# Optimization experiments

Measured on AMD Instinct MI355X. Metric: run time of the kernel, lower is better.

The kernel has to match this reference:

```python
import jax, jax.numpy as jnp
import numpy as np

B, H, W, C = 8, 64, 64, 256  # NHWC, SAGAN-style feature map


def setup_inputs() -> dict:
    key = jax.random.key(0)
    ks = jax.random.split(key, 10)
    d_qk, d_v = C // 8, C // 2
    sc = lambda fan_in: 1.0 / np.sqrt(fan_in)
    return {
        "x": jax.random.normal(ks[0], (B, H, W, C), dtype=jnp.float32),
        "Wf": jax.random.normal(ks[1], (C, d_qk), dtype=jnp.float32) * sc(C),
        "bf": jnp.zeros((d_qk,), dtype=jnp.float32),
        "Wg": jax.random.normal(ks[2], (C, d_qk), dtype=jnp.float32) * sc(C),
        "bg": jnp.zeros((d_qk,), dtype=jnp.float32),
        "Wh": jax.random.normal(ks[3], (C, d_v), dtype=jnp.float32) * sc(C),
        "bh": jnp.zeros((d_v,), dtype=jnp.float32),
        "Wo": jax.random.normal(ks[4], (d_v, C), dtype=jnp.float32) * sc(d_v),
        "bo": jnp.zeros((C,), dtype=jnp.float32),
        # original inits gamma=0.0 (identity fwd); use nonzero so fwd exercises attention
        "gamma": jnp.float32(0.5),
    }


def reference(x, Wf, bf, Wg, bg, Wh, bh, Wo, bo, gamma):
    b, h_, w_, c = x.shape
    n = h_ * w_
    xf = x.reshape(b, n, c)  # 1x1 convs are per-pixel GEMMs
    f = xf @ Wf + bf          # [B, N, C/8]  (keys)
    g = xf @ Wg + bg          # [B, N, C/8]  (queries)
    hv = xf @ Wh + bh         # [B, N, C/2]  (values)
    s = jnp.einsum('bnd,bmd->bnm', g, f)   # unscaled scores [B, N, N]
    beta = jax.nn.softmax(s, axis=-1)
    o = jnp.einsum('bnm,bmd->bnd', beta, hv)  # [B, N, C/2]
    o = o @ Wo + bo                           # output 1x1 conv -> [B, N, C]
    out = gamma * o + xf
    return out.reshape(b, h_, w_, c)
```

## Files before the change

### kernel.cpp

```cpp
#include <hip/hip_runtime.h>
#include <hip/hip_bf16.h>

#define NB   8
#define CC   256
#define NN   4096
#define NTOT (NB*NN)
#define DQK  32
#define DV   128

typedef __attribute__((ext_vector_type(8))) short bf16x8;
typedef __attribute__((ext_vector_type(4))) short s16x4;
typedef __attribute__((ext_vector_type(4))) float f32x4;
typedef __attribute__((ext_vector_type(16))) float f32x16;
typedef __attribute__((ext_vector_type(4))) float float4v;
typedef __attribute__((ext_vector_type(4))) unsigned int u32x4;

__device__ __forceinline__ short f2bf(float f) {
    __hip_bfloat16 h = __float2bfloat16(f);
    return *reinterpret_cast<short*>(&h);
}
__device__ __forceinline__ float bf2f(short s) {
    unsigned int u = ((unsigned int)(unsigned short)s) << 16;
    return __builtin_bit_cast(float, u);
}
__device__ __forceinline__ unsigned int cvtpk(float lo, float hi) {
    unsigned int r;
    asm("v_cvt_pk_bf16_f32 %0, %1, %2" : "=v"(r) : "v"(lo), "v"(hi));
    return r;
}
__device__ __forceinline__ void plswap(unsigned int &a, unsigned int &b) {
    asm("v_permlane32_swap_b32 %0, %1" : "+v"(a), "+v"(b));
}

#define OFF_F     0u
#define OFF_G     (2u<<20)
#define OFF_VT    (4u<<20)
#define OFF_OP    (12u<<20)
#define OFF_LS    (28u<<20)
#define OFF_WQKVT ((28u<<20)+(512u<<10))
#define OFF_WOT   (OFF_WQKVT + 192u*256u*2u)

__global__ __launch_bounds__(256) void prep_kernel(
    const float* __restrict__ Wf, const float* __restrict__ Wg,
    const float* __restrict__ Wh, const float* __restrict__ Wo,
    short* __restrict__ WqkvT, short* __restrict__ WoT)
{
    int idx = blockIdx.x * 256 + threadIdx.x;
    if (idx < 192 * 256) {
        int j = idx >> 8, k = idx & 255;
        float v = (j < 32) ? Wf[k * 32 + j]
                : (j < 64) ? Wg[k * 32 + (j - 32)]
                           : Wh[k * 128 + (j - 64)];
        WqkvT[j * 256 + k] = f2bf(v);
    }
    int i2 = idx - 192 * 256;
    if (i2 >= 0 && i2 < 256 * 128) {
        int c = i2 >> 7, d = i2 & 127;
        WoT[c * 128 + d] = f2bf(Wo[d * 256 + c]);
    }
}

__global__ __launch_bounds__(256) void proj_kernel(
    const float* __restrict__ x,
    const float* __restrict__ bf_, const float* __restrict__ bg_,
    const float* __restrict__ bh_,
    const short* __restrict__ WqkvT,
    short* __restrict__ fws, short* __restrict__ gws, short* __restrict__ vtile)
{
    __shared__ short hlds[128 * 72];

    int wid = threadIdx.x >> 6, lane = threadIdx.x & 63;
    int col16 = lane & 15, rq = lane >> 4;
    int bid = blockIdx.x;
    int sid = (bid & 7) * 64 + (bid >> 3);
    int nloc = wid * 16 + col16;
    int arow = sid * 64 + nloc;
    int b = sid >> 6, kt = sid & 63;

    f32x4 acc[12];
    #pragma unroll
    for (int i = 0; i < 12; ++i) acc[i] = (f32x4){0.f, 0.f, 0.f, 0.f};

    const float* xrow = x + (size_t)arow * CC;
    #pragma unroll
    for (int kk = 0; kk < 8; ++kk) {
        int k0 = kk * 32 + rq * 8;
        float4v u0 = *(const float4v*)(xrow + k0);
        float4v u1 = *(const float4v*)(xrow + k0 + 4);
        bf16x8 av;
        av[0]=f2bf(u0[0]); av[1]=f2bf(u0[1]); av[2]=f2bf(u0[2]); av[3]=f2bf(u0[3]);
        av[4]=f2bf(u1[0]); av[5]=f2bf(u1[1]); av[6]=f2bf(u1[2]); av[7]=f2bf(u1[3]);
        #pragma unroll
        for (int nf = 0; nf < 12; ++nf) {
            bf16x8 bv = *(const bf16x8*)(WqkvT + (nf * 16 + col16) * 256 + k0);
            acc[nf] = __builtin_amdgcn_mfma_f32_16x16x32_bf16(bv, av, acc[nf], 0, 0, 0);
        }
    }

    #pragma unroll
    for (int nf = 0; nf < 2; ++nf) {
        int c0 = nf * 16 + rq * 4;
        float4v b4 = *(const float4v*)(bf_ + c0);
        s16x4 v = { f2bf(acc[nf][0] + b4[0]), f2bf(acc[nf][1] + b4[1]),
                    f2bf(acc[nf][2] + b4[2]), f2bf(acc[nf][3] + b4[3]) };
        *(s16x4*)(fws + (size_t)arow * DQK + c0) = v;
    }
    #pragma unroll
    for (int nf = 2; nf < 4; ++nf) {
        int c0 = (nf - 2) * 16 + rq * 4;
        float4v b4 = *(const float4v*)(bg_ + c0);
        s16x4 v = { f2bf((acc[nf][0] + b4[0]) * 1.44269504089f),
                    f2bf((acc[nf][1] + b4[1]) * 1.44269504089f),
                    f2bf((acc[nf][2] + b4[2]) * 1.44269504089f),
                    f2bf((acc[nf][3] + b4[3]) * 1.44269504089f) };
        *(s16x4*)(gws + (size_t)arow * DQK + c0) = v;
    }

    #pragma unroll
    for (int nf = 4; nf < 12; ++nf) {
        int d0 = (nf - 4) * 16 + rq * 4;
        float4v b4 = *(const float4v*)(bh_ + d0);
        #pragma unroll
        for (int r = 0; r < 4; ++r)
            hlds[(d0 + r) * 72 + nloc] = f2bf(acc[nf][r] + b4[r]);
    }
    __syncthreads();

    int t = threadIdx.x;
    int l31 = t & 31, dt = (t >> 5) & 3, klh = t >> 7;
    int d = dt * 32 + l31;
    #pragma unroll
    for (int kslot = 0; kslot < 4; ++kslot) {
        bf16x8 v = *(const bf16x8*)(&hlds[d * 72 + kslot * 16 + klh * 8]);
        size_t addr = (((size_t)(b * 64 + kt) * 4 + kslot) * 2048)
                    + dt * 512 + klh * 256 + l31 * 8;
        *(bf16x8*)(vtile + addr) = v;
    }
}

__global__ __launch_bounds__(256, 4) void attn_kernel(
    const short* __restrict__ fws, const short* __restrict__ gws,
    const short* __restrict__ vtile, short* __restrict__ opart,
    float* __restrict__ lspart)
{
    __shared__ __align__(16) char smem[33280];

    int t = threadIdx.x;
    int wid = t >> 6, lane = t & 63;
    int l31 = lane & 31, lh = lane >> 5;
    int qh = wid >> 1, kh = wid & 1;

    int bid = blockIdx.x;
    int sid = (bid & 7) * 128 + (bid >> 3);
    int b = sid >> 7, rem = sid & 127;
    int ksh = rem >> 6, qt = rem & 63;
    int qbase = b * NN + qt * 64;
    int k0 = ksh * 32, kend = k0 + 32;

    const short* grow = gws + (size_t)(qbase + qh * 32 + l31) * DQK;
    bf16x8 gb0 = *(const bf16x8*)(grow + lh * 8);
    bf16x8 gb1 = *(const bf16x8*)(grow + 16 + lh * 8);

    int foff = (kh * 32 + l31) * DQK + lh * 8;
    const short* fS = fws + (size_t)b * NN * DQK;

    f32x16 oaccT[4], zero16;
    #pragma unroll
    for (int i = 0; i < 16; ++i) {
        zero16[i] = 0.f;
        oaccT[0][i] = 0.f; oaccT[1][i] = 0.f; oaccT[2][i] = 0.f; oaccT[3][i] = 0.f;
    }
    float lsum = 0.f;

    bf16x8 fc0 = *(const bf16x8*)(fS + (size_t)k0 * 2048 + foff);
    bf16x8 fc1 = *(const bf16x8*)(fS + (size_t)k0 * 2048 + foff + 16);

    for (int kb = k0; kb < kend; ++kb) {
        const short* fnp = fS + (size_t)(kb + 1) * 2048 + foff;
        bf16x8 fn0 = *(const bf16x8*)(fnp);
        bf16x8 fn1 = *(const bf16x8*)(fnp + 16);

        f32x16 s = __builtin_amdgcn_mfma_f32_32x32x16_bf16(fc0, gb0, zero16, 0, 0, 0);
        s = __builtin_amdgcn_mfma_f32_32x32x16_bf16(fc1, gb1, s, 0, 0, 0);

        unsigned int w[8];
        #pragma unroll
        for (int i = 0; i < 8; ++i) {
            float pa = __builtin_exp2f(s[2 * i]);
            float pb = __builtin_exp2f(s[2 * i + 1]);
            lsum += pa + pb;
            w[i] = cvtpk(pa, pb);
        }
        plswap(w[0], w[2]); plswap(w[1], w[3]);
        plswap(w[4], w[6]); plswap(w[5], w[7]);

        const short* vb_kb = vtile + (((size_t)(b * 64 + kb) * 4 + kh * 2) * 2048)
                           + (size_t)lane * 8;
        #pragma unroll
        for (int ks = 0; ks < 2; ++ks) {
            u32x4 pw = { w[ks * 4], w[ks * 4 + 1], w[ks * 4 + 2], w[ks * 4 + 3] };
            bf16x8 pb_ = __builtin_bit_cast(bf16x8, pw);
            #pragma unroll
            for (int dt = 0; dt < 4; ++dt) {
                bf16x8 va = *(const bf16x8*)(vb_kb + ks * 2048 + dt * 512);
                oaccT[dt] = __builtin_amdgcn_mfma_f32_32x32x16_bf16(va, pb_, oaccT[dt], 0, 0, 0);
            }
        }
        fc0 = fn0; fc1 = fn1;
    }

    lsum += __shfl_xor(lsum, 32);
    float* lsbuf = (float*)(&smem[32768]);
    if (lh == 0) lsbuf[(qh * 2 + kh) * 32 + l31] = lsum;
    __syncthreads();

    char* obuf = smem;
    if (kh == 1) {
        #pragma unroll
        for (int dt = 0; dt < 4; ++dt) {
            #pragma unroll
            for (int r = 0; r < 16; ++r) {
                int d = dt * 32 + (r & 3) + 8 * (r >> 2) + 4 * lh;
                int q = qh * 32 + l31;
                int byte = q * 512 + ((((d >> 2) ^ (q & 31)) << 4) | ((d & 3) << 2));
                *(float*)(obuf + byte) = oaccT[dt][r];
            }
        }
    }
    __syncthreads();
    if (kh == 0) {
        float tot = lsbuf[qh * 64 + l31] + lsbuf[qh * 64 + 32 + l31];
        if (lh == 0) lspart[(size_t)(qbase + qh * 32 + l31) * 2 + ksh] = tot;
        float iv = 1.f / tot;
        #pragma unroll
        for (int dt = 0; dt < 4; ++dt) {
            #pragma unroll
            for (int r = 0; r < 16; ++r) {
                int d = dt * 32 + (r & 3) + 8 * (r >> 2) + 4 * lh;
                int q = qh * 32 + l31;
                int byte = q * 512 + ((((d >> 2) ^ (q & 31)) << 4) | ((d & 3) << 2));
                float* p = (float*)(obuf + byte);
                *p = (*p + oaccT[dt][r]) * iv;
            }
        }
    }
    __syncthreads();
    {
        int q = t >> 2, dg = t & 3;
        size_t orow = ((size_t)(qbase + q) * 2 + ksh) * 128 + dg * 32;
        #pragma unroll
        for (int cc = 0; cc < 8; cc += 2) {
            int c0 = dg * 8 + cc;
            f32x4 u0 = *(const f32x4*)(obuf + q * 512 + (((c0 ^ (q & 31)) << 4)));
            f32x4 u1 = *(const f32x4*)(obuf + q * 512 + ((((c0 + 1) ^ (q & 31)) << 4)));
            bf16x8 ov;
            ov[0]=f2bf(u0[0]); ov[1]=f2bf(u0[1]); ov[2]=f2bf(u0[2]); ov[3]=f2bf(u0[3]);
            ov[4]=f2bf(u1[0]); ov[5]=f2bf(u1[1]); ov[6]=f2bf(u1[2]); ov[7]=f2bf(u1[3]);
            *(bf16x8*)(opart + orow + cc * 4) = ov;
        }
    }
}

__global__ __launch_bounds__(256) void out_kernel(
    const short* __restrict__ opart, const float* __restrict__ lspart,
    const short* __restrict__ WoT,
    const float* __restrict__ bo, const float* __restrict__ gamma,
    const float* __restrict__ x, float* __restrict__ out)
{
    int wid = threadIdx.x >> 6, lane = threadIdx.x & 63;
    int col16 = lane & 15, rq = lane >> 4;
    int bid = blockIdx.x;
    int sid = (bid & 7) * 128 + (bid >> 3);
    int rh = wid & 1, ch = wid >> 1;
    int arow = sid * 32 + rh * 16 + col16;

    float l0 = lspart[(size_t)arow * 2];
    float l1 = lspart[(size_t)arow * 2 + 1];
    float iv = 1.f / (l0 + l1);
    float w0 = l0 * iv, w1 = l1 * iv;

    const short* oprow = opart + (size_t)arow * 256;
    bf16x8 bfr[4];
    #pragma unroll
    for (int kk = 0; kk < 4; ++kk) {
        bf16x8 a0 = *(const bf16x8*)(oprow + kk * 32 + rq * 8);
        bf16x8 a1 = *(const bf16x8*)(oprow + 128 + kk * 32 + rq * 8);
        bf16x8 af;
        #pragma unroll
        for (int j = 0; j < 8; ++j)
            af[j] = f2bf(w0 * bf2f(a0[j]) + w1 * bf2f(a1[j]));
        bfr[kk] = af;
    }

    f32x4 acc[8];
    #pragma unroll
    for (int i = 0; i < 8; ++i) acc[i] = (f32x4){0.f, 0.f, 0.f, 0.f};

    #pragma unroll
    for (int nf = 0; nf < 8; ++nf) {
        int nt = ch * 8 + nf;
        #pragma unroll
        for (int kk = 0; kk < 4; ++kk) {
            bf16x8 wfr = *(const bf16x8*)(WoT + (nt * 16 + col16) * DV + kk * 32 + rq * 8);
            acc[nf] = __builtin_amdgcn_mfma_f32_16x16x32_bf16(wfr, bfr[kk], acc[nf], 0, 0, 0);
        }
    }

    float gm = gamma[0];
    const float* xrow = x + (size_t)arow * CC;
    float* orow_ = out + (size_t)arow * CC;
    #pragma unroll
    for (int nf = 0; nf < 8; ++nf) {
        int c0 = (ch * 8 + nf) * 16 + rq * 4;
        float4v bo4 = *(const float4v*)(bo + c0);
        float4v xv = *(const float4v*)(xrow + c0);
        float4v ov;
        #pragma unroll
        for (int r = 0; r < 4; ++r)
            ov[r] = gm * (acc[nf][r] + bo4[r]) + xv[r];
        *(float4v*)(orow_ + c0) = ov;
    }
}

extern "C" void kernel_launch(void* const* d_in, const int* in_sizes, int n_in,
                              void* d_out, int out_size, void* d_ws, size_t ws_size,
                              hipStream_t stream)
{
    const float* x     = (const float*)d_in[0];
    const float* Wf    = (const float*)d_in[1];
    const float* bf_   = (const float*)d_in[2];
    const float* Wg    = (const float*)d_in[3];
    const float* bg_   = (const float*)d_in[4];
    const float* Wh    = (const float*)d_in[5];
    const float* bh_   = (const float*)d_in[6];
    const float* Wo    = (const float*)d_in[7];
    const float* bo    = (const float*)d_in[8];
    const float* gamma = (const float*)d_in[9];

    char* ws = (char*)d_ws;
    short* fws   = (short*)(ws + OFF_F);
    short* gws   = (short*)(ws + OFF_G);
    short* vtile = (short*)(ws + OFF_VT);
    short* opart = (short*)(ws + OFF_OP);
    float* lsp   = (float*)(ws + OFF_LS);
    short* WqkvT = (short*)(ws + OFF_WQKVT);
    short* WoT   = (short*)(ws + OFF_WOT);
    float* out   = (float*)d_out;

    hipLaunchKernelGGL(prep_kernel, dim3(320), dim3(256), 0, stream, Wf, Wg, Wh, Wo, WqkvT, WoT);
    hipLaunchKernelGGL(proj_kernel, dim3(512), dim3(256), 0, stream,
                       x, bf_, bg_, bh_, WqkvT, fws, gws, vtile);
    hipLaunchKernelGGL(attn_kernel, dim3(1024), dim3(256), 0, stream, fws, gws, vtile, opart, lsp);
    hipLaunchKernelGGL(out_kernel, dim3(1024), dim3(256), 0, stream, opart, lsp, WoT, bo, gamma, x, out);
}
```

Measured before the change: 126.0 us.

## Split projection over 32-row tiles with column halves per wave; use packed bf16 converts

```diff
diff --git a/kernel.cpp b/kernel.cpp
--- a/kernel.cpp
+++ b/kernel.cpp
@@ -14,6 +14,7 @@
 typedef __attribute__((ext_vector_type(16))) float f32x16;
 typedef __attribute__((ext_vector_type(4))) float float4v;
 typedef __attribute__((ext_vector_type(4))) unsigned int u32x4;
+typedef __attribute__((ext_vector_type(2))) unsigned int u32x2;
 
 __device__ __forceinline__ short f2bf(float f) {
     __hip_bfloat16 h = __float2bfloat16(f);
@@ -67,19 +68,21 @@
     const short* __restrict__ WqkvT,
     short* __restrict__ fws, short* __restrict__ gws, short* __restrict__ vtile)
 {
-    __shared__ short hlds[128 * 72];
+    __shared__ short hlds[128 * 40];
 
     int wid = threadIdx.x >> 6, lane = threadIdx.x & 63;
     int col16 = lane & 15, rq = lane >> 4;
     int bid = blockIdx.x;
-    int sid = (bid & 7) * 64 + (bid >> 3);
-    int nloc = wid * 16 + col16;
-    int arow = sid * 64 + nloc;
-    int b = sid >> 6, kt = sid & 63;
-
-    f32x4 acc[12];
-    #pragma unroll
-    for (int i = 0; i < 12; ++i) acc[i] = (f32x4){0.f, 0.f, 0.f, 0.f};
+    int sid = (bid & 7) * 128 + (bid >> 3);
+    int b = sid >> 7, nt = sid & 127;
+    int rh = wid & 1, ch = wid >> 1;
+    int nloc = rh * 16 + col16;
+    int arow = sid * 32 + nloc;
+    int kt = nt >> 1, ksb = (nt & 1) * 2;
+
+    f32x4 acc[6];
+    #pragma unroll
+    for (int i = 0; i < 6; ++i) acc[i] = (f32x4){0.f, 0.f, 0.f, 0.f};
 
     const float* xrow = x + (size_t)arow * CC;
     #pragma unroll
@@ -87,54 +90,72 @@
         int k0 = kk * 32 + rq * 8;
         float4v u0 = *(const float4v*)(xrow + k0);
         float4v u1 = *(const float4v*)(xrow + k0 + 4);
-        bf16x8 av;
-        av[0]=f2bf(u0[0]); av[1]=f2bf(u0[1]); av[2]=f2bf(u0[2]); av[3]=f2bf(u0[3]);
-        av[4]=f2bf(u1[0]); av[5]=f2bf(u1[1]); av[6]=f2bf(u1[2]); av[7]=f2bf(u1[3]);
-        #pragma unroll
-        for (int nf = 0; nf < 12; ++nf) {
-            bf16x8 bv = *(const bf16x8*)(WqkvT + (nf * 16 + col16) * 256 + k0);
+        u32x4 avw = { cvtpk(u0[0], u0[1]), cvtpk(u0[2], u0[3]),
+                      cvtpk(u1[0], u1[1]), cvtpk(u1[2], u1[3]) };
+        bf16x8 av = __builtin_bit_cast(bf16x8, avw);
+        #pragma unroll
+        for (int nf = 0; nf < 6; ++nf) {
+            int ct = ch * 6 + nf;
+            bf16x8 bv = *(const bf16x8*)(WqkvT + (ct * 16 + col16) * 256 + k0);
             acc[nf] = __builtin_amdgcn_mfma_f32_16x16x32_bf16(bv, av, acc[nf], 0, 0, 0);
         }
     }
 
-    #pragma unroll
-    for (int nf = 0; nf < 2; ++nf) {
-        int c0 = nf * 16 + rq * 4;
-        float4v b4 = *(const float4v*)(bf_ + c0);
-        s16x4 v = { f2bf(acc[nf][0] + b4[0]), f2bf(acc[nf][1] + b4[1]),
-                    f2bf(acc[nf][2] + b4[2]), f2bf(acc[nf][3] + b4[3]) };
-        *(s16x4*)(fws + (size_t)arow * DQK + c0) = v;
-    }
-    #pragma unroll
-    for (int nf = 2; nf < 4; ++nf) {
-        int c0 = (nf - 2) * 16 + rq * 4;
-        float4v b4 = *(const float4v*)(bg_ + c0);
-        s16x4 v = { f2bf((acc[nf][0] + b4[0]) * 1.44269504089f),
-                    f2bf((acc[nf][1] + b4[1]) * 1.44269504089f),
-                    f2bf((acc[nf][2] + b4[2]) * 1.44269504089f),
-                    f2bf((acc[nf][3] + b4[3]) * 1.44269504089f) };
-        *(s16x4*)(gws + (size_t)arow * DQK + c0) = v;
-    }
-
-    #pragma unroll
-    for (int nf = 4; nf < 12; ++nf) {
-        int d0 = (nf - 4) * 16 + rq * 4;
-        float4v b4 = *(const float4v*)(bh_ + d0);
-        #pragma unroll
-        for (int r = 0; r < 4; ++r)
-            hlds[(d0 + r) * 72 + nloc] = f2bf(acc[nf][r] + b4[r]);
+    if (ch == 0) {
+        #pragma unroll
+        for (int nf = 0; nf < 2; ++nf) {
+            int c0 = nf * 16 + rq * 4;
+            float4v b4 = *(const float4v*)(bf_ + c0);
+            u32x2 v = { cvtpk(acc[nf][0] + b4[0], acc[nf][1] + b4[1]),
+                        cvtpk(acc[nf][2] + b4[2], acc[nf][3] + b4[3]) };
+            *(u32x2*)(fws + (size_t)arow * DQK + c0) = v;
+        }
+        #pragma unroll
+        for (int nf = 2; nf < 4; ++nf) {
+            int c0 = (nf - 2) * 16 + rq * 4;
+            float4v b4 = *(const float4v*)(bg_ + c0);
+            u32x2 v = { cvtpk((acc[nf][0] + b4[0]) * 1.44269504089f,
+                              (acc[nf][1] + b4[1]) * 1.44269504089f),
+                        cvtpk((acc[nf][2] + b4[2]) * 1.44269504089f,
+                              (acc[nf][3] + b4[3]) * 1.44269504089f) };
+            *(u32x2*)(gws + (size_t)arow * DQK + c0) = v;
+        }
+        #pragma unroll
+        for (int nf = 4; nf < 6; ++nf) {
+            int d0 = (nf - 4) * 16 + rq * 4;
+            float4v b4 = *(const float4v*)(bh_ + d0);
+            unsigned int p01 = cvtpk(acc[nf][0] + b4[0], acc[nf][1] + b4[1]);
+            unsigned int p23 = cvtpk(acc[nf][2] + b4[2], acc[nf][3] + b4[3]);
+            hlds[(d0 + 0) * 40 + nloc] = (short)(p01 & 0xffff);
+            hlds[(d0 + 1) * 40 + nloc] = (short)(p01 >> 16);
+            hlds[(d0 + 2) * 40 + nloc] = (short)(p23 & 0xffff);
+            hlds[(d0 + 3) * 40 + nloc] = (short)(p23 >> 16);
+        }
+    } else {
+        #pragma unroll
+        for (int nf = 0; nf < 6; ++nf) {
+            int d0 = (nf + 2) * 16 + rq * 4;
+            float4v b4 = *(const float4v*)(bh_ + d0);
+            unsigned int p01 = cvtpk(acc[nf][0] + b4[0], acc[nf][1] + b4[1]);
+            unsigned int p23 = cvtpk(acc[nf][2] + b4[2], acc[nf][3] + b4[3]);
+            hlds[(d0 + 0) * 40 + nloc] = (short)(p01 & 0xffff);
+            hlds[(d0 + 1) * 40 + nloc] = (short)(p01 >> 16);
+            hlds[(d0 + 2) * 40 + nloc] = (short)(p23 & 0xffff);
+            hlds[(d0 + 3) * 40 + nloc] = (short)(p23 >> 16);
+        }
     }
     __syncthreads();
 
     int t = threadIdx.x;
-    int l31 = t & 31, dt = (t >> 5) & 3, klh = t >> 7;
-    int d = dt * 32 + l31;
-    #pragma unroll
-    for (int kslot = 0; kslot < 4; ++kslot) {
-        bf16x8 v = *(const bf16x8*)(&hlds[d * 72 + kslot * 16 + klh * 8]);
-        size_t addr = (((size_t)(b * 64 + kt) * 4 + kslot) * 2048)
-                    + dt * 512 + klh * 256 + l31 * 8;
-        *(bf16x8*)(vtile + addr) = v;
+    #pragma unroll
+    for (int i = 0; i < 2; ++i) {
+        int v = i * 256 + t;
+        int d = v >> 2, g = v & 3;
+        bf16x8 vec = *(const bf16x8*)(&hlds[d * 40 + g * 8]);
+        int ks = ksb + (g >> 1), klh = g & 1;
+        size_t addr = (((size_t)(b * 64 + kt) * 4 + ks) * 2048)
+                    + (d >> 5) * 512 + klh * 256 + (d & 31) * 8;
+        *(bf16x8*)(vtile + addr) = vec;
     }
 }
 
@@ -285,11 +306,13 @@
     for (int kk = 0; kk < 4; ++kk) {
         bf16x8 a0 = *(const bf16x8*)(oprow + kk * 32 + rq * 8);
         bf16x8 a1 = *(const bf16x8*)(oprow + 128 + kk * 32 + rq * 8);
-        bf16x8 af;
+        float m[8];
         #pragma unroll
         for (int j = 0; j < 8; ++j)
-            af[j] = f2bf(w0 * bf2f(a0[j]) + w1 * bf2f(a1[j]));
-        bfr[kk] = af;
+            m[j] = w0 * bf2f(a0[j]) + w1 * bf2f(a1[j]);
+        u32x4 wv = { cvtpk(m[0], m[1]), cvtpk(m[2], m[3]),
+                     cvtpk(m[4], m[5]), cvtpk(m[6], m[7]) };
+        bfr[kk] = __builtin_bit_cast(bf16x8, wv);
     }
 
     f32x4 acc[8];
@@ -348,7 +371,7 @@
     float* out   = (float*)d_out;
 
     hipLaunchKernelGGL(prep_kernel, dim3(320), dim3(256), 0, stream, Wf, Wg, Wh, Wo, WqkvT, WoT);
-    hipLaunchKernelGGL(proj_kernel, dim3(512), dim3(256), 0, stream,
+    hipLaunchKernelGGL(proj_kernel, dim3(1024), dim3(256), 0, stream,
                        x, bf_, bg_, bh_, WqkvT, fws, gws, vtile);
     hipLaunchKernelGGL(attn_kernel, dim3(1024), dim3(256), 0, stream, fws, gws, vtile, opart, lsp);
     hipLaunchKernelGGL(out_kernel, dim3(1024), dim3(256), 0, stream, opart, lsp, WoT, bo, gamma, x, out);
```

New measurement: 129.1 us. 1.02x slower.
